# Kernel tuning notes

Hardware: AMD Instinct MI355X
Metric: run time of the kernel (lower is better)

## Reference

```python
import jax, jax.numpy as jnp
import numpy as np

T, B, H, L = 1024, 64, 512, 2  # seq_len, batch, hidden(=input), num_layers


def setup_inputs() -> dict:
    key = jax.random.key(0)
    ks = jax.random.split(key, 9)
    std = 1.0 / np.sqrt(H)

    def u(k, shape):
        return jax.random.uniform(k, shape, jnp.float32, -std, std)

    x = jax.random.normal(ks[0], (T, B, H), jnp.float32)
    # per-direction stacked params: weights [L, 4H, in], biases [L, 4H]
    Wxh_f = u(ks[1], (L, 4 * H, H)); bxh_f = u(ks[2], (L, 4 * H))
    Whh_f = u(ks[3], (L, 4 * H, H)); bhh_f = u(ks[4], (L, 4 * H))
    Wxh_b = u(ks[5], (L, 4 * H, H)); bxh_b = u(ks[6], (L, 4 * H))
    Whh_b = u(ks[7], (L, 4 * H, H)); bhh_b = u(ks[8], (L, 4 * H))
    # LSTMCell.reset_parameters sets forget-gate bias chunk to 1/H
    fg = 1.0 / H
    bxh_f = bxh_f.at[:, H:2 * H].set(fg); bhh_f = bhh_f.at[:, H:2 * H].set(fg)
    bxh_b = bxh_b.at[:, H:2 * H].set(fg); bhh_b = bhh_b.at[:, H:2 * H].set(fg)
    return {"x": x,
            "Wxh_f": Wxh_f, "bxh_f": bxh_f, "Whh_f": Whh_f, "bhh_f": bhh_f,
            "Wxh_b": Wxh_b, "bxh_b": bxh_b, "Whh_b": Whh_b, "bhh_b": bhh_b}


def _run_direction(x, Wxh, bxh, Whh, bhh, reverse):
    # x: [T, B, in]; stacked L-layer LSTM scan in one direction.
    seq = x
    hs, cs = [], []
    for l in range(L):
        Wx, bx, Wh, bh = Wxh[l], bxh[l], Whh[l], bhh[l]

        def step(carry, xt):
            h, c = carry
            g = xt @ Wx.T + bx + h @ Wh.T + bh  # [B, 4H]
            i, f, gc, o = jnp.split(g, 4, axis=-1)  # chunk order: i, f, c, o
            c2 = jax.nn.sigmoid(f) * c + jax.nn.sigmoid(i) * jnp.tanh(gc)
            h2 = jax.nn.sigmoid(o) * jnp.tanh(c2)
            return (h2, c2), h2

        z = jnp.zeros((x.shape[1], H), x.dtype)
        (h, c), seq = jax.lax.scan(step, (z, z), seq, reverse=reverse)
        hs.append(h); cs.append(c)
    return seq, jnp.stack(hs), jnp.stack(cs)  # [T,B,H], [L,B,H], [L,B,H]


def reference(x, Wxh_f, bxh_f, Whh_f, bhh_f, Wxh_b, bxh_b, Whh_b, bhh_b):
    out_f, h_f, c_f = _run_direction(x, Wxh_f, bxh_f, Whh_f, bhh_f, reverse=False)
    out_b, h_b, c_b = _run_direction(x, Wxh_b, bxh_b, Whh_b, bhh_b, reverse=True)
    output = jnp.concatenate([out_f, out_b], axis=-1)  # [T, B, 2H]
    hidden = jnp.concatenate([h_f, h_b], axis=0)       # [2L, B, H]
    cell = jnp.concatenate([c_f, c_b], axis=0)         # [2L, B, H]
    return (output, hidden, cell)
```

## Files before the change

### kernel.cpp

```cpp
#include <hip/hip_runtime.h>
#include <hip/hip_bf16.h>


typedef __hip_bfloat16 bf16;
typedef short bf16x8 __attribute__((ext_vector_type(8)));
typedef float f32x4 __attribute__((ext_vector_type(4)));
typedef unsigned long long u64;

constexpr int T = 1024, B = 64, H = 512, G4 = 2048;
constexpr int W = 16;
constexpr int NW = 64;
constexpr int FSTRIDE = 16;
constexpr size_t OUT_ELEMS = (size_t)T * B * 1024;
constexpr size_t HID_OFF   = OUT_ELEMS;
constexpr size_t CELL_OFF  = OUT_ELEMS + (size_t)4 * B * H;

__device__ __align__(256) unsigned g_flags[4 * NW * FSTRIDE];
__device__ __align__(256) bf16 g_ring [2 * W * B * H];
__device__ __align__(256) bf16 g_ring2[2 * W * B * H];

__global__ void init_ctrs() {
  const int i = blockIdx.x * blockDim.x + threadIdx.x;
  if (i < 4 * NW * FSTRIDE) g_flags[i] = 0;
}

__device__ __forceinline__ bf16x8 cvt8(const float* p) {
  const float4 u = *(const float4*)p;
  const float4 v = *(const float4*)(p + 4);
  union { bf16 h[8]; bf16x8 r; } o;
  o.h[0] = __float2bfloat16(u.x); o.h[1] = __float2bfloat16(u.y);
  o.h[2] = __float2bfloat16(u.z); o.h[3] = __float2bfloat16(u.w);
  o.h[4] = __float2bfloat16(v.x); o.h[5] = __float2bfloat16(v.y);
  o.h[6] = __float2bfloat16(v.z); o.h[7] = __float2bfloat16(v.w);
  return o.r;
}

__device__ __forceinline__ bf16x8 ld16_dev(const bf16* p) {
  union { u64 u[2]; bf16x8 v; } r;
  r.u[0] = __hip_atomic_load((const u64*)p,     __ATOMIC_RELAXED,
                             __HIP_MEMORY_SCOPE_AGENT);
  r.u[1] = __hip_atomic_load((const u64*)p + 1, __ATOMIC_RELAXED,
                             __HIP_MEMORY_SCOPE_AGENT);
  return r.v;
}

__device__ __forceinline__ void st2_dev(bf16* p, float x) {
  const bf16 h = (bf16)x;
  unsigned short u;
  __builtin_memcpy(&u, &h, 2);
  __hip_atomic_store((unsigned short*)p, u, __ATOMIC_RELAXED,
                     __HIP_MEMORY_SCOPE_AGENT);
}

__device__ __forceinline__ void wave_poll(const unsigned* base, int lane,
                                          unsigned tgt) {
  const unsigned* p = base + lane * FSTRIDE;
  for (;;) {
    unsigned v = __hip_atomic_load(p, __ATOMIC_RELAXED,
                                   __HIP_MEMORY_SCOPE_AGENT);
    if (__all((int)(v >= tgt))) break;
    __builtin_amdgcn_s_sleep(1);
  }
}

__global__ void __launch_bounds__(256, 1)
lstm_bidir(const float* __restrict__ x,
           const float* Wxf, const float* bxf, const float* Whf, const float* bhf,
           const float* Wxb, const float* bxb, const float* Whb, const float* bhb,
           float* out)
{
  __shared__ bf16 Wl[32 * 1024];

  const int tid   = threadIdx.x;
  const int bid   = blockIdx.x;
  const int stage = bid & 3;
  const int wg    = bid >> 2;
  const int dir   = stage & 1;
  const int layer = stage >> 1;
  const int c0    = wg * 8;

  const float* Wx = dir ? Wxb : Wxf;
  const float* Wh = dir ? Whb : Whf;
  const float* bx = dir ? bxb : bxf;
  const float* bh = dir ? bhb : bhf;
  bf16* ring  = g_ring  + (size_t)dir * W * B * H;
  bf16* ring2 = g_ring2 + (size_t)dir * W * B * H;

  for (int c = tid; c < 32 * 128; c += 256) {
    const int n  = c >> 7;
    const int kb = c & 127;
    const int ke = kb * 8;
    const int j = n >> 2, g = n & 3;
    const size_t row = (size_t)layer * G4 + (size_t)g * H + (c0 + j);
    const float* src = (ke < H) ? (Wx + row * H + ke) : (Wh + row * H + (ke - H));
    bf16x8 wv = cvt8(src);
    *(bf16x8*)(Wl + n * 1024 + ((kb ^ (n & 7)) * 8)) = wv;
  }

  const int lane = tid & 63, wi = tid >> 6;
  const int quad = lane >> 4, mr = lane & 15;
  const int g2 = wi & 1;
  const int mh = wi >> 1;
  const int nb = g2 * 16 + mr;
  const int j  = nb >> 2, gg = nb & 3;
  const int sw = nb & 7;

  const size_t brow = (size_t)layer * G4 + (size_t)gg * H + (c0 + j);
  const float bias = bx[brow] + bh[brow];

  __syncthreads();

  float cst[2][4] = {};
  unsigned nrounds = 0;
  unsigned*       myflags   = g_flags + stage * NW * FSTRIDE;
  const unsigned* prodflags = g_flags + dir * NW * FSTRIDE;
  const unsigned* consflags = g_flags + (2 + dir) * NW * FSTRIDE;

  const int r0 = (stage < 2) ? 0 : 1;
  for (int r = r0; r < r0 + T; ++r) {
    int t;
    if (stage == 0)      t = r;
    else if (stage == 1) t = (T - 1) - r;
    else if (stage == 2) t = r - 1;
    else                 t = T - r;

    const bool first = dir ? (t == T - 1) : (t == 0);
    const bool last  = dir ? (t == 0) : (t == T - 1);

    const float* xf = nullptr;
    const bf16 *xsb = nullptr;
    const bf16 *hsrc; bf16* hdst_bf; float* hdst_f32 = nullptr;
    if (stage < 2) {
      xf      = x    + (size_t)t * B * H;
      hsrc    = ring + (size_t)((r - 1) & (W - 1)) * B * H;
      hdst_bf = ring + (size_t)(r & (W - 1)) * B * H;
    } else {
      xsb      = ring  + (size_t)((r - 1) & (W - 1)) * B * H;
      hsrc     = ring2 + (size_t)((r - 1) & (W - 1)) * B * H;
      hdst_bf  = ring2 + (size_t)(r & (W - 1)) * B * H;
      hdst_f32 = out + (size_t)t * B * 1024 + (size_t)dir * H;
    }

    f32x4 acc0 = {0.f, 0.f, 0.f, 0.f};
    f32x4 acc1 = {0.f, 0.f, 0.f, 0.f};
    const int arow = mh * 32 + mr;

    if (stage < 2) {
      #pragma unroll
      for (int kk = 0; kk < 16; ++kk) {
        const int blk = kk * 4 + quad;
        bf16x8 bfr = *(const bf16x8*)(Wl + nb * 1024 + ((blk ^ sw) * 8));
        const float* ap = xf + (size_t)arow * H + blk * 8;
        bf16x8 a0 = cvt8(ap);
        bf16x8 a1 = cvt8(ap + (size_t)16 * H);
        acc0 = __builtin_amdgcn_mfma_f32_16x16x32_bf16(a0, bfr, acc0, 0, 0, 0);
        acc1 = __builtin_amdgcn_mfma_f32_16x16x32_bf16(a1, bfr, acc1, 0, 0, 0);
      }
      if (!first) {
        #pragma unroll
        for (int kk = 0; kk < 16; ++kk) {
          const int blk = 64 + kk * 4 + quad;
          bf16x8 bfr = *(const bf16x8*)(Wl + nb * 1024 + ((blk ^ sw) * 8));
          const bf16* ap = hsrc + (size_t)arow * H + (kk * 4 + quad) * 8;
          bf16x8 a0 = ld16_dev(ap);
          bf16x8 a1 = ld16_dev(ap + (size_t)16 * H);
          acc0 = __builtin_amdgcn_mfma_f32_16x16x32_bf16(a0, bfr, acc0, 0, 0, 0);
          acc1 = __builtin_amdgcn_mfma_f32_16x16x32_bf16(a1, bfr, acc1, 0, 0, 0);
        }
      }
      if (r >= W) {
        if (tid < 64) wave_poll(consflags, tid, (unsigned)(r - W + 1));
        __syncthreads();
      }
    } else {
      if (!first) {
        #pragma unroll
        for (int kk = 0; kk < 16; ++kk) {
          const int blk = 64 + kk * 4 + quad;
          bf16x8 bfr = *(const bf16x8*)(Wl + nb * 1024 + ((blk ^ sw) * 8));
          const bf16* ap = hsrc + (size_t)arow * H + (kk * 4 + quad) * 8;
          bf16x8 a0 = ld16_dev(ap);
          bf16x8 a1 = ld16_dev(ap + (size_t)16 * H);
          acc0 = __builtin_amdgcn_mfma_f32_16x16x32_bf16(a0, bfr, acc0, 0, 0, 0);
          acc1 = __builtin_amdgcn_mfma_f32_16x16x32_bf16(a1, bfr, acc1, 0, 0, 0);
        }
      }
      if (tid < 64) wave_poll(prodflags, tid, (unsigned)r);
      __syncthreads();
      #pragma unroll
      for (int kk = 0; kk < 16; ++kk) {
        const int blk = kk * 4 + quad;
        bf16x8 bfr = *(const bf16x8*)(Wl + nb * 1024 + ((blk ^ sw) * 8));
        const bf16* ap = xsb + (size_t)arow * H + blk * 8;
        bf16x8 a0 = ld16_dev(ap);
        bf16x8 a1 = ld16_dev(ap + (size_t)16 * H);
        acc0 = __builtin_amdgcn_mfma_f32_16x16x32_bf16(a0, bfr, acc0, 0, 0, 0);
        acc1 = __builtin_amdgcn_mfma_f32_16x16x32_bf16(a1, bfr, acc1, 0, 0, 0);
      }
    }

    #pragma unroll
    for (int m = 0; m < 2; ++m) {
      const f32x4 av = m ? acc1 : acc0;
      #pragma unroll
      for (int rr = 0; rr < 4; ++rr) {
        const float v  = av[rr] + bias;
        const float v1 = __shfl_xor(v, 1);
        const float v2 = __shfl_xor(v, 2);
        const float v3 = __shfl_xor(v, 3);
        float gi, gf, gc, go;
        if (gg == 0)      { gi = v;  gf = v1; gc = v2; go = v3; }
        else if (gg == 1) { gi = v1; gf = v;  gc = v3; go = v2; }
        else if (gg == 2) { gi = v2; gf = v3; gc = v;  go = v1; }
        else              { gi = v3; gf = v2; gc = v1; go = v;  }
        const float si = 1.f / (1.f + __expf(-gi));
        const float sf = 1.f / (1.f + __expf(-gf));
        const float so = 1.f / (1.f + __expf(-go));
        const float tc = 1.f - 2.f / (1.f + __expf(2.f * gc));
        const float c2 = sf * cst[m][rr] + si * tc;
        cst[m][rr] = c2;
        const float th = 1.f - 2.f / (1.f + __expf(2.f * c2));
        const float hv = so * th;
        if (gg == 0) {
          const int b = mh * 32 + m * 16 + quad * 4 + rr;
          st2_dev(hdst_bf + (size_t)b * H + (c0 + j), hv);
          if (stage >= 2) hdst_f32[(size_t)b * 1024 + (c0 + j)] = hv;
          if (last) {
            const size_t p = (size_t)(dir * 2 + layer) * (B * H) + (size_t)b * H + (c0 + j);
            out[HID_OFF + p]  = hv;
            out[CELL_OFF + p] = c2;
          }
        }
      }
    }

    asm volatile("s_waitcnt vmcnt(0)" ::: "memory");
    __syncthreads();
    ++nrounds;
    if (tid < 64) {
      if (tid == 0) {
        __hip_atomic_store(myflags + wg * FSTRIDE, nrounds,
                           __ATOMIC_RELAXED, __HIP_MEMORY_SCOPE_AGENT);
      }
      wave_poll(myflags, tid, nrounds);
    }
    __syncthreads();
  }
}

extern "C" void kernel_launch(void* const* d_in, const int* in_sizes, int n_in,
                              void* d_out, int out_size, void* d_ws, size_t ws_size,
                              hipStream_t stream) {
  const float* x   = (const float*)d_in[0];
  const float* Wxf = (const float*)d_in[1];
  const float* bxf = (const float*)d_in[2];
  const float* Whf = (const float*)d_in[3];
  const float* bhf = (const float*)d_in[4];
  const float* Wxb = (const float*)d_in[5];
  const float* bxb = (const float*)d_in[6];
  const float* Whb = (const float*)d_in[7];
  const float* bhb = (const float*)d_in[8];
  float* out = (float*)d_out;

  hipLaunchKernelGGL(init_ctrs, dim3(16), dim3(256), 0, stream);
  hipLaunchKernelGGL(lstm_bidir, dim3(256), dim3(256), 0, stream,
                     x, Wxf, bxf, Whf, bhf, Wxb, bxb, Whb, bhb, out);
}
```

Baseline: 19.50 ms.

## Replace per-stage all-to-all barrier with leader-aggregated epoch counters

Drops the end-of-step wait in which every workgroup polled all 64 peer flags. Now workgroup 0 of each stage gathers the flags and publishes a single epoch counter, and the other workgroups poll only that one word. The barrier moves to just before the recurrent h-matmul, so the x-projection (layer 0) or the cross-layer input projection (layer 1) runs before the wait instead of after it. Consumers and producers also sync through the epoch counters instead of scanning full flag arrays. This cuts polling traffic and hides latency, at the cost of an extra hop through the leader and a final epoch publish after the loop.

```diff
diff --git a/kernel.cpp b/kernel.cpp
--- a/kernel.cpp
+++ b/kernel.cpp
@@ -11,17 +11,20 @@
 constexpr int W = 16;
 constexpr int NW = 64;
 constexpr int FSTRIDE = 16;
+constexpr int ESTRIDE = 16;
 constexpr size_t OUT_ELEMS = (size_t)T * B * 1024;
 constexpr size_t HID_OFF   = OUT_ELEMS;
 constexpr size_t CELL_OFF  = OUT_ELEMS + (size_t)4 * B * H;
 
 __device__ __align__(256) unsigned g_flags[4 * NW * FSTRIDE];
+__device__ __align__(256) unsigned g_epoch[4 * ESTRIDE];
 __device__ __align__(256) bf16 g_ring [2 * W * B * H];
 __device__ __align__(256) bf16 g_ring2[2 * W * B * H];
 
 __global__ void init_ctrs() {
   const int i = blockIdx.x * blockDim.x + threadIdx.x;
   if (i < 4 * NW * FSTRIDE) g_flags[i] = 0;
+  if (i < 4 * ESTRIDE)      g_epoch[i] = 0;
 }
 
 __device__ __forceinline__ bf16x8 cvt8(const float* p) {
@@ -61,6 +64,12 @@
     if (__all((int)(v >= tgt))) break;
     __builtin_amdgcn_s_sleep(1);
   }
+}
+
+__device__ __forceinline__ void poll_ge(const unsigned* p, unsigned tgt) {
+  while (__hip_atomic_load(p, __ATOMIC_RELAXED,
+                           __HIP_MEMORY_SCOPE_AGENT) < tgt)
+    __builtin_amdgcn_s_sleep(1);
 }
 
 __global__ void __launch_bounds__(256, 1)
@@ -113,8 +122,9 @@
   float cst[2][4] = {};
   unsigned nrounds = 0;
   unsigned*       myflags   = g_flags + stage * NW * FSTRIDE;
-  const unsigned* prodflags = g_flags + dir * NW * FSTRIDE;
-  const unsigned* consflags = g_flags + (2 + dir) * NW * FSTRIDE;
+  unsigned*       myepoch   = g_epoch + stage * ESTRIDE;
+  const unsigned* prodepoch = g_epoch + dir * ESTRIDE;
+  const unsigned* consepoch = g_epoch + (2 + dir) * ESTRIDE;
 
   const int r0 = (stage < 2) ? 0 : 1;
   for (int r = r0; r < r0 + T; ++r) {
@@ -156,6 +166,20 @@
         acc0 = __builtin_amdgcn_mfma_f32_16x16x32_bf16(a0, bfr, acc0, 0, 0, 0);
         acc1 = __builtin_amdgcn_mfma_f32_16x16x32_bf16(a1, bfr, acc1, 0, 0, 0);
       }
+      if (tid < 64) {
+        if (wg == 0) {
+          wave_poll(myflags, tid, nrounds);
+          if (tid == 0) {
+            __hip_atomic_store(myepoch, nrounds, __ATOMIC_RELAXED,
+                               __HIP_MEMORY_SCOPE_AGENT);
+            if (r >= W) poll_ge(consepoch, (unsigned)(r - W + 1));
+          }
+        } else if (tid == 0) {
+          poll_ge(myepoch, nrounds);
+          if (r >= W) poll_ge(consepoch, (unsigned)(r - W + 1));
+        }
+      }
+      __syncthreads();
       if (!first) {
         #pragma unroll
         for (int kk = 0; kk < 16; ++kk) {
@@ -168,11 +192,30 @@
           acc1 = __builtin_amdgcn_mfma_f32_16x16x32_bf16(a1, bfr, acc1, 0, 0, 0);
         }
       }
-      if (r >= W) {
-        if (tid < 64) wave_poll(consflags, tid, (unsigned)(r - W + 1));
-        __syncthreads();
-      }
     } else {
+      if (tid == 0) poll_ge(prodepoch, (unsigned)r);
+      __syncthreads();
+      #pragma unroll
+      for (int kk = 0; kk < 16; ++kk) {
+        const int blk = kk * 4 + quad;
+        bf16x8 bfr = *(const bf16x8*)(Wl + nb * 1024 + ((blk ^ sw) * 8));
+        const bf16* ap = xsb + (size_t)arow * H + blk * 8;
+        bf16x8 a0 = ld16_dev(ap);
+        bf16x8 a1 = ld16_dev(ap + (size_t)16 * H);
+        acc0 = __builtin_amdgcn_mfma_f32_16x16x32_bf16(a0, bfr, acc0, 0, 0, 0);
+        acc1 = __builtin_amdgcn_mfma_f32_16x16x32_bf16(a1, bfr, acc1, 0, 0, 0);
+      }
+      if (tid < 64) {
+        if (wg == 0) {
+          wave_poll(myflags, tid, nrounds);
+          if (tid == 0)
+            __hip_atomic_store(myepoch, nrounds, __ATOMIC_RELAXED,
+                               __HIP_MEMORY_SCOPE_AGENT);
+        } else if (tid == 0) {
+          poll_ge(myepoch, nrounds);
+        }
+      }
+      __syncthreads();
       if (!first) {
         #pragma unroll
         for (int kk = 0; kk < 16; ++kk) {
@@ -184,18 +227,6 @@
           acc0 = __builtin_amdgcn_mfma_f32_16x16x32_bf16(a0, bfr, acc0, 0, 0, 0);
           acc1 = __builtin_amdgcn_mfma_f32_16x16x32_bf16(a1, bfr, acc1, 0, 0, 0);
         }
-      }
-      if (tid < 64) wave_poll(prodflags, tid, (unsigned)r);
-      __syncthreads();
-      #pragma unroll
-      for (int kk = 0; kk < 16; ++kk) {
-        const int blk = kk * 4 + quad;
-        bf16x8 bfr = *(const bf16x8*)(Wl + nb * 1024 + ((blk ^ sw) * 8));
-        const bf16* ap = xsb + (size_t)arow * H + blk * 8;
-        bf16x8 a0 = ld16_dev(ap);
-        bf16x8 a1 = ld16_dev(ap + (size_t)16 * H);
-        acc0 = __builtin_amdgcn_mfma_f32_16x16x32_bf16(a0, bfr, acc0, 0, 0, 0);
-        acc1 = __builtin_amdgcn_mfma_f32_16x16x32_bf16(a1, bfr, acc1, 0, 0, 0);
       }
     }
 
@@ -237,14 +268,17 @@
     asm volatile("s_waitcnt vmcnt(0)" ::: "memory");
     __syncthreads();
     ++nrounds;
-    if (tid < 64) {
-      if (tid == 0) {
-        __hip_atomic_store(myflags + wg * FSTRIDE, nrounds,
-                           __ATOMIC_RELAXED, __HIP_MEMORY_SCOPE_AGENT);
-      }
-      wave_poll(myflags, tid, nrounds);
+    if (tid == 0) {
+      __hip_atomic_store(myflags + wg * FSTRIDE, nrounds,
+                         __ATOMIC_RELAXED, __HIP_MEMORY_SCOPE_AGENT);
     }
-    __syncthreads();
+  }
+
+  if (wg == 0 && tid < 64) {
+    wave_poll(myflags, tid, (unsigned)T);
+    if (tid == 0)
+      __hip_atomic_store(myepoch, (unsigned)T, __ATOMIC_RELAXED,
+                         __HIP_MEMORY_SCOPE_AGENT);
   }
 }
 
```

After: 18.92 ms. 2.9% less time.
